# Kernel optimization log

Hardware: AMD Instinct MI355X
Metric: run time of the kernel (lower is better)

The kernel has to match this reference:

```python
import jax, jax.numpy as jnp
import numpy as np

B, S, V, D, H, DK, DH, L = 1, 2048, 256, 1024, 16, 64, 4096, 4
EPS = 1e-5
SCALE = 1.0 / np.sqrt(DK)


def _ln(x, g, b):
    mu = jnp.mean(x, axis=-1, keepdims=True)
    var = jnp.mean(jnp.square(x - mu), axis=-1, keepdims=True)
    return (x - mu) * jax.lax.rsqrt(var + EPS) * g + b


def setup_inputs() -> dict:
    key = jax.random.key(0)
    ks = jax.random.split(key, 20)
    f = lambda k, shape: (0.02 * jax.random.normal(k, shape)).astype(jnp.float32)
    return {
        "x": jax.random.randint(ks[0], (B, S), 0, V),
        "emb": f(ks[1], (V, D)),
        "pos": f(ks[2], (S, D)),
        "Wq": f(ks[3], (L, D, H * DK)), "bq": jnp.zeros((L, H * DK), jnp.float32),
        "Wk": f(ks[4], (L, D, H * DK)), "bk": jnp.zeros((L, H * DK), jnp.float32),
        "Wv": f(ks[5], (L, D, H * DK)), "bv": jnp.zeros((L, H * DK), jnp.float32),
        "Wo": f(ks[6], (L, H * DK, D)),
        "ln1_g": jnp.ones((L, D), jnp.float32), "ln1_b": jnp.zeros((L, D), jnp.float32),
        "W1": f(ks[7], (L, D, DH)), "b1": jnp.zeros((L, DH), jnp.float32),
        "W2": f(ks[8], (L, DH, D)), "b2": jnp.zeros((L, D), jnp.float32),
        "ln2_g": jnp.ones((L, D), jnp.float32), "ln2_b": jnp.zeros((L, D), jnp.float32),
        "head_w": f(ks[9], (D, V)), "head_b": jnp.zeros((V,), jnp.float32),
    }


def _forward(x, emb, pos, Wq, bq, Wk, bk, Wv, bv, Wo, ln1_g, ln1_b,
             W1, b1, W2, b2, ln2_g, ln2_b, head_w, head_b):
    h = emb[x] + pos[:S]                      # [B,S,D]
    causal = jnp.tril(jnp.ones((S, S), bool))  # additive -inf above diag
    for i in range(L):
        # --- naive attention: explicit QK^T, mask, softmax, @V ---
        q = (h @ Wq[i] + bq[i]).reshape(B, S, H, DK)
        k = (h @ Wk[i] + bk[i]).reshape(B, S, H, DK)
        v = (h @ Wv[i] + bv[i]).reshape(B, S, H, DK)
        scores = jnp.einsum('bqhd,bkhd->bhqk', q * SCALE, k)   # [B,H,S,S]
        scores = jnp.where(causal[None, None], scores, -jnp.inf)
        p = jax.nn.softmax(scores, axis=-1)
        a = jnp.einsum('bhqk,bkhd->bqhd', p, v).reshape(B, S, H * DK) @ Wo[i]
        # --- TransformerLayer: x + ln2(mlp(x + ln1(attn(x)))) ---
        u = h + _ln(a, ln1_g[i], ln1_b[i])
        m = jax.nn.gelu(u @ W1[i] + b1[i], approximate=False) @ W2[i] + b2[i]
        h = h + _ln(m, ln2_g[i], ln2_b[i])
    return h @ head_w + head_b                 # [B,S,V]


def reference(x, emb, pos, Wq, bq, Wk, bk, Wv, bv, Wo, ln1_g, ln1_b,
              W1, b1, W2, b2, ln2_g, ln2_b, head_w, head_b):
    return _forward(x, emb, pos, Wq, bq, Wk, bk, Wv, bv, Wo, ln1_g, ln1_b,
                    W1, b1, W2, b2, ln2_g, ln2_b, head_w, head_b)
```

## Files before the change

kernel.cpp:

```cpp
#include <hip/hip_runtime.h>
#include <hip/hip_bf16.h>
#include <cstdint>
#include <math.h>

static constexpr int S_  = 2048;
static constexpr int D_  = 1024;
static constexpr int H_  = 16;
static constexpr int DK_ = 64;
static constexpr int DH_ = 4096;
static constexpr int L_  = 4;
static constexpr int V_  = 256;
#define ATT_SCALE 0.125f

typedef __bf16 bf16;
typedef __bf16 bf16x8 __attribute__((ext_vector_type(8)));
typedef __bf16 bf16x4v __attribute__((ext_vector_type(4)));
typedef float  f32x4  __attribute__((ext_vector_type(4)));

__device__ __forceinline__ __attribute__((address_space(3))) void* to_lds(const void* p) {
  return (__attribute__((address_space(3))) void*)(uintptr_t)p;
}
__device__ __forceinline__ __attribute__((address_space(1))) void* to_glb(const void* p) {
  return (__attribute__((address_space(1))) void*)(uintptr_t)p;
}

template <int TN, int SPLIT, int GELU_EPI>
__device__ __forceinline__ void gemm_body(
    const bf16* __restrict__ A, const bf16* __restrict__ Bt,
    const float* __restrict__ bias, float* __restrict__ Cf, bf16* __restrict__ Cb,
    float* __restrict__ P0, float* __restrict__ P1,
    int M, int N, int K)
{
  constexpr int BU = TN / 32;
  constexpr int JN = TN / 32;
  __shared__ __align__(16) bf16 sA[2][128 * 64];
  __shared__ __align__(16) bf16 sB[2][TN * 64];
  const int tid  = threadIdx.x;
  const int wave = tid >> 6;
  const int lane = tid & 63;
  const int l16  = lane & 15;
  const int quad = lane >> 4;

  const int idl = blockIdx.y * 16 + blockIdx.x;
  const int qch = (gridDim.x * gridDim.y) >> 3;
  const int wsw = (idl & 7) * qch + (idl >> 3);
  const int bm  = (wsw & 15) * 128;
  const int bn  = (wsw >> 4) * TN;

  const int wm = (wave & 1) * 64;
  const int wn = (wave >> 1) * (TN / 2);

  const int KS = K / SPLIT;
  const size_t kofs = (SPLIT > 1) ? (size_t)blockIdx.z * KS : 0;

  const int srow = tid >> 3;
  const int sc8  = (tid & 7) ^ (srow & 7);
  const bf16* gA = A  + (size_t)(bm + srow) * K + kofs + sc8 * 8;
  const bf16* gB = Bt + (size_t)(bn + srow) * K + kofs + sc8 * 8;

  const int swz = l16 & 7;

  f32x4 acc[4][JN] = {};

#pragma unroll
  for (int u = 0; u < 4; ++u)
    __builtin_amdgcn_global_load_lds(to_glb(gA + (size_t)u * 32 * K),
                                     to_lds(&sA[0][u * 2048 + tid * 8]), 16, 0, 0);
#pragma unroll
  for (int u = 0; u < BU; ++u)
    __builtin_amdgcn_global_load_lds(to_glb(gB + (size_t)u * 32 * K),
                                     to_lds(&sB[0][u * 2048 + tid * 8]), 16, 0, 0);

  int cur = 0;
  for (int k0 = 0; k0 < KS; k0 += 64, cur ^= 1) {
    if (k0 + 64 < KS) {
      const int nb = cur ^ 1;
      const size_t ko = k0 + 64;
#pragma unroll
      for (int u = 0; u < 4; ++u)
        __builtin_amdgcn_global_load_lds(to_glb(gA + ko + (size_t)u * 32 * K),
                                         to_lds(&sA[nb][u * 2048 + tid * 8]), 16, 0, 0);
#pragma unroll
      for (int u = 0; u < BU; ++u)
        __builtin_amdgcn_global_load_lds(to_glb(gB + ko + (size_t)u * 32 * K),
                                         to_lds(&sB[nb][u * 2048 + tid * 8]), 16, 0, 0);
      if constexpr (BU == 4) asm volatile("s_waitcnt vmcnt(8)" ::: "memory");
      else                   asm volatile("s_waitcnt vmcnt(6)" ::: "memory");
    } else {
      asm volatile("s_waitcnt vmcnt(0)" ::: "memory");
    }
    __builtin_amdgcn_s_barrier();

    bf16x8 af[2][4], bfv[2][JN];
#pragma unroll
    for (int kc = 0; kc < 2; ++kc) {
      const int c8 = ((kc * 4 + quad) ^ swz) * 8;
#pragma unroll
      for (int i = 0; i < 4; ++i)
        af[kc][i] = *(const bf16x8*)&sA[cur][(wm + i * 16 + l16) * 64 + c8];
#pragma unroll
      for (int j = 0; j < JN; ++j)
        bfv[kc][j] = *(const bf16x8*)&sB[cur][(wn + j * 16 + l16) * 64 + c8];
    }
    asm volatile("s_waitcnt lgkmcnt(0)" ::: "memory");
    __builtin_amdgcn_s_barrier();

#pragma unroll
    for (int kc = 0; kc < 2; ++kc)
#pragma unroll
      for (int i = 0; i < 4; ++i)
#pragma unroll
        for (int j = 0; j < JN; ++j)
          acc[i][j] = __builtin_amdgcn_mfma_f32_16x16x32_bf16(af[kc][i], bfv[kc][j], acc[i][j], 0, 0, 0);
  }

  if constexpr (SPLIT > 1) {
    float* Pf;
    if constexpr (SPLIT == 4)
      Pf = (blockIdx.z < 2) ? (P0 + (size_t)blockIdx.z * ((size_t)M * N))
                            : (P1 + (size_t)(blockIdx.z - 2) * ((size_t)M * N));
    else
      Pf = (blockIdx.z == 0) ? P0 : P1;
#pragma unroll
    for (int i = 0; i < 4; ++i)
#pragma unroll
      for (int j = 0; j < JN; ++j) {
        const int col = bn + wn + j * 16 + l16;
#pragma unroll
        for (int r = 0; r < 4; ++r) {
          const int row = bm + wm + i * 16 + quad * 4 + r;
          Pf[(size_t)row * N + col] = acc[i][j][r];
        }
      }
  } else {
#pragma unroll
    for (int i = 0; i < 4; ++i) {
#pragma unroll
      for (int j = 0; j < JN; ++j) {
        const int col = bn + wn + j * 16 + l16;
        const float bz = bias ? bias[col] : 0.0f;
#pragma unroll
        for (int r = 0; r < 4; ++r) {
          const int row = bm + wm + i * 16 + quad * 4 + r;
          float v = acc[i][j][r] + bz;
          if (GELU_EPI) v = 0.5f * v * (1.0f + erff(v * 0.70710678118654752f));
          if (Cf) Cf[(size_t)row * N + col] = v;
          if (Cb) Cb[(size_t)row * N + col] = (bf16)v;
        }
      }
    }
  }
}

__global__ __launch_bounds__(256) void gemm_qkv_kernel(
    const bf16* __restrict__ A, const bf16* __restrict__ Bt,
    const float* __restrict__ bias, bf16* __restrict__ Cb, int M, int N, int K)
{ gemm_body<64, 1, 0>(A, Bt, bias, nullptr, Cb, nullptr, nullptr, M, N, K); }

__global__ __launch_bounds__(256) void gemm_wo_kernel(
    const bf16* __restrict__ A, const bf16* __restrict__ Bt,
    float* __restrict__ P0, float* __restrict__ P1, int M, int N, int K)
{ gemm_body<128, 2, 0>(A, Bt, nullptr, nullptr, nullptr, P0, P1, M, N, K); }

__global__ __launch_bounds__(256) void gemm_mlp1_kernel(
    const bf16* __restrict__ A, const bf16* __restrict__ Bt,
    const float* __restrict__ bias, bf16* __restrict__ Cb, int M, int N, int K)
{ gemm_body<64, 1, 1>(A, Bt, bias, nullptr, Cb, nullptr, nullptr, M, N, K); }

__global__ __launch_bounds__(256) void gemm_mlp2_kernel(
    const bf16* __restrict__ A, const bf16* __restrict__ Bt,
    float* __restrict__ P0, float* __restrict__ P1, int M, int N, int K)
{ gemm_body<128, 4, 0>(A, Bt, nullptr, nullptr, nullptr, P0, P1, M, N, K); }

__global__ __launch_bounds__(256) void gemm_head_kernel(
    const bf16* __restrict__ A, const bf16* __restrict__ Bt,
    float* __restrict__ P0, float* __restrict__ P1, int M, int N, int K)
{ gemm_body<64, 4, 0>(A, Bt, nullptr, nullptr, nullptr, P0, P1, M, N, K); }

__global__ __launch_bounds__(256) void splitk_reduce4_kernel(
    const float* __restrict__ P0, const float* __restrict__ P1,
    const float* __restrict__ bias, float* __restrict__ Cf, size_t MN, int N)
{
  const size_t i = ((size_t)blockIdx.x * 256 + threadIdx.x) * 4;
  const float4 a = *(const float4*)(P0 + i);
  const float4 b = *(const float4*)(P0 + MN + i);
  const float4 c = *(const float4*)(P1 + i);
  const float4 d = *(const float4*)(P1 + MN + i);
  float4 o;
  o.x = a.x + b.x + c.x + d.x; o.y = a.y + b.y + c.y + d.y;
  o.z = a.z + b.z + c.z + d.z; o.w = a.w + b.w + c.w + d.w;
  const int col = (int)(i & (size_t)(N - 1));
  const float4 bz = *(const float4*)(bias + col);
  o.x += bz.x; o.y += bz.y; o.z += bz.z; o.w += bz.w;
  *(float4*)(Cf + i) = o;
}

__device__ __forceinline__ float wave_reduce_sum(float v) {
#pragma unroll
  for (int off = 32; off > 0; off >>= 1) v += __shfl_xor(v, off, 64);
  return v;
}

template <int SPLIT>
__device__ __forceinline__ void ln_fused_body(
    const float* __restrict__ P0, const float* __restrict__ P1,
    const float* __restrict__ bias, const float* __restrict__ resid,
    const float* __restrict__ g, const float* __restrict__ b,
    float* __restrict__ outf, bf16* __restrict__ outb, size_t MN)
{
  const int r = blockIdx.x;
  const int t = threadIdx.x;
  const size_t ro = (size_t)r * D_;
  float4 x;
  {
    const float4 a0 = ((const float4*)(P0 + ro))[t];
    float4 a1;
    if constexpr (SPLIT == 2) a1 = ((const float4*)(P1 + ro))[t];
    else                      a1 = ((const float4*)(P0 + MN + ro))[t];
    x.x = a0.x + a1.x; x.y = a0.y + a1.y; x.z = a0.z + a1.z; x.w = a0.w + a1.w;
    if constexpr (SPLIT == 4) {
      const float4 a2 = ((const float4*)(P1 + ro))[t];
      const float4 a3 = ((const float4*)(P1 + MN + ro))[t];
      x.x += a2.x + a3.x; x.y += a2.y + a3.y; x.z += a2.z + a3.z; x.w += a2.w + a3.w;
    }
  }
  if (bias) {
    const float4 bz = ((const float4*)bias)[t];
    x.x += bz.x; x.y += bz.y; x.z += bz.z; x.w += bz.w;
  }
  float s  = x.x + x.y + x.z + x.w;
  float s2 = x.x * x.x + x.y * x.y + x.z * x.z + x.w * x.w;
  s  = wave_reduce_sum(s);
  s2 = wave_reduce_sum(s2);
  __shared__ float red[8];
  const int wave = t >> 6, lane = t & 63;
  if (lane == 0) { red[wave] = s; red[4 + wave] = s2; }
  __syncthreads();
  s  = red[0] + red[1] + red[2] + red[3];
  s2 = red[4] + red[5] + red[6] + red[7];
  const float mu  = s * (1.0f / 1024.0f);
  const float var = s2 * (1.0f / 1024.0f) - mu * mu;
  const float rs  = rsqrtf(var + 1e-5f);
  const float4 gv = ((const float4*)g)[t];
  const float4 bv = ((const float4*)b)[t];
  const float4 hv = ((const float4*)(resid + ro))[t];
  const float o0 = hv.x + (x.x - mu) * rs * gv.x + bv.x;
  const float o1 = hv.y + (x.y - mu) * rs * gv.y + bv.y;
  const float o2 = hv.z + (x.z - mu) * rs * gv.z + bv.z;
  const float o3 = hv.w + (x.w - mu) * rs * gv.w + bv.w;
  if (outf) { float4 o4; o4.x = o0; o4.y = o1; o4.z = o2; o4.w = o3;
              ((float4*)(outf + ro))[t] = o4; }
  if (outb) { bf16x4v ob = {(bf16)o0, (bf16)o1, (bf16)o2, (bf16)o3};
              ((bf16x4v*)(outb + ro))[t] = ob; }
}

__global__ __launch_bounds__(256) void ln_fused2_kernel(
    const float* __restrict__ P0, const float* __restrict__ P1,
    const float* __restrict__ resid, const float* __restrict__ g,
    const float* __restrict__ b, bf16* __restrict__ outb, size_t MN)
{ ln_fused_body<2>(P0, P1, nullptr, resid, g, b, nullptr, outb, MN); }

__global__ __launch_bounds__(256) void ln_fused4_kernel(
    const float* __restrict__ P0, const float* __restrict__ P1,
    const float* __restrict__ bias, const float* __restrict__ resid,
    const float* __restrict__ g, const float* __restrict__ b,
    float* __restrict__ outf, bf16* __restrict__ outb, size_t MN)
{ ln_fused_body<4>(P0, P1, bias, resid, g, b, outf, outb, MN); }

__device__ __forceinline__ void transpose_tile(
    const float* __restrict__ in, bf16* __restrict__ out, int K, int N)
{
  __shared__ float t[32][33];
  const int k0 = blockIdx.y * 32;
  const int n0 = blockIdx.x * 32;
  const int tx = threadIdx.x & 31;
  const int ty = threadIdx.x >> 5;
#pragma unroll
  for (int i = 0; i < 32; i += 8)
    t[ty + i][tx] = in[(size_t)(k0 + ty + i) * N + (n0 + tx)];
  __syncthreads();
#pragma unroll
  for (int i = 0; i < 32; i += 8)
    out[(size_t)(n0 + ty + i) * K + (k0 + tx)] = (bf16)t[tx][ty + i];
}

__global__ __launch_bounds__(256) void transpose_cast_kernel(
    const float* __restrict__ in, bf16* __restrict__ out, int K, int N)
{ transpose_tile(in, out, K, N); }

__global__ __launch_bounds__(256) void transpose_all_kernel(
    const float* __restrict__ in, bf16* __restrict__ out, int K, int N,
    size_t in_stride, size_t out_stride)
{
  transpose_tile(in + (size_t)blockIdx.z * in_stride,
                 out + (size_t)blockIdx.z * out_stride, K, N);
}

__global__ __launch_bounds__(256) void transpose_qkv_all_kernel(
    const float* __restrict__ Wq, const float* __restrict__ Wk, const float* __restrict__ Wv,
    bf16* __restrict__ out)
{
  const int z = blockIdx.z;
  const int layer = z / 3, which = z % 3;
  const float* in = (which == 0) ? Wq : (which == 1) ? Wk : Wv;
  transpose_tile(in + (size_t)layer * D_ * D_,
                 out + ((size_t)layer * 3 + which) * D_ * D_, D_, D_);
}

__global__ __launch_bounds__(256) void vtrans_kernel(
    const bf16* __restrict__ qkv, bf16* __restrict__ vT)
{
  __shared__ bf16 t[32][65];
  const int s0 = blockIdx.x * 32;
  const int head = blockIdx.y;
  const int sr = threadIdx.x >> 3, d8 = (threadIdx.x & 7) * 8;
  bf16x8 v = *(const bf16x8*)(qkv + (size_t)(s0 + sr) * (3 * D_) + 2 * D_ + head * DK_ + d8);
#pragma unroll
  for (int i = 0; i < 8; ++i) t[sr][d8 + i] = v[i];
  __syncthreads();
  const int dw = threadIdx.x >> 2, s4 = (threadIdx.x & 3) * 8;
  bf16x8 o;
#pragma unroll
  for (int i = 0; i < 8; ++i) o[i] = t[s4 + i][dw];
  *(bf16x8*)(vT + (size_t)head * DK_ * S_ + (size_t)dw * S_ + s0 + s4) = o;
}

__global__ __launch_bounds__(256) void embed_kernel(
    const int* __restrict__ x, const float* __restrict__ emb, const float* __restrict__ pos,
    float* __restrict__ hf, bf16* __restrict__ hb)
{
  const int s = blockIdx.x;
  const int d = threadIdx.x * 4;
  const int tok = x[s];
  const float4 e = *(const float4*)(emb + (size_t)tok * D_ + d);
  const float4 p = *(const float4*)(pos + (size_t)s * D_ + d);
  float4 o; o.x = e.x + p.x; o.y = e.y + p.y; o.z = e.z + p.z; o.w = e.w + p.w;
  *(float4*)(hf + (size_t)s * D_ + d) = o;
  bf16x4v ob = {(bf16)o.x, (bf16)o.y, (bf16)o.z, (bf16)o.w};
  *(bf16x4v*)(hb + (size_t)s * D_ + d) = ob;
}

__global__ __launch_bounds__(256) void attn_mfma_kernel(
    const bf16* __restrict__ qkv, const bf16* __restrict__ vT, bf16* __restrict__ out)
{
  __shared__ __align__(16) bf16 sK[2][64 * 64];
  __shared__ __align__(16) bf16 sV[2][64 * 64];
  __shared__ __align__(16) bf16 sP[4][16 * 64];

  const int head = blockIdx.y;
  const int xb   = blockIdx.x;
  const int qIdx = (head & 8) ? (31 - xb) : xb;
  const int qb   = qIdx * 64;
  const int tid  = threadIdx.x;
  const int wave = tid >> 6, lane = tid & 63;
  const int l16  = lane & 15, quad = lane >> 4;
  const int swz  = l16 & 7;

  const size_t rstr = 3 * D_;
  const bf16* kbase = qkv + D_ + head * DK_;
  const bf16* vbase = vT + (size_t)head * DK_ * S_;

  const int srow   = tid >> 3;
  const int kchunk = (tid & 7) ^ (srow & 7);

  bf16x8 aq0, aq1;
  {
    const bf16* qrow = qkv + (size_t)(qb + wave * 16 + l16) * rstr + head * DK_ + quad * 8;
    bf16x8 t0 = *(const bf16x8*)(qrow);
    bf16x8 t1 = *(const bf16x8*)(qrow + 32);
#pragma unroll
    for (int i = 0; i < 8; ++i) {
      aq0[i] = (bf16)((float)t0[i] * ATT_SCALE);
      aq1[i] = (bf16)((float)t1[i] * ATT_SCALE);
    }
  }

  f32x4 oa[4] = {};
  float lsum[4] = {0.0f, 0.0f, 0.0f, 0.0f};
  const int qrow0 = qb + wave * 16 + quad * 4;
  const int jmax = qb + 63;

#pragma unroll
  for (int u = 0; u < 2; ++u) {
    const int r = u * 32 + srow;
    __builtin_amdgcn_global_load_lds(to_glb(kbase + (size_t)r * rstr + kchunk * 8),
                                     to_lds(&sK[0][u * 2048 + tid * 8]), 16, 0, 0);
    __builtin_amdgcn_global_load_lds(to_glb(vbase + (size_t)r * S_ + kchunk * 8),
                                     to_lds(&sV[0][u * 2048 + tid * 8]), 16, 0, 0);
  }

  int cur = 0;
  for (int j0 = 0; j0 <= jmax; j0 += 64, cur ^= 1) {
    if (j0 + 64 <= jmax) {
      const int nb = cur ^ 1;
      const int jn = j0 + 64;
#pragma unroll
      for (int u = 0; u < 2; ++u) {
        const int r = u * 32 + srow;
        __builtin_amdgcn_global_load_lds(to_glb(kbase + (size_t)(jn + r) * rstr + kchunk * 8),
                                         to_lds(&sK[nb][u * 2048 + tid * 8]), 16, 0, 0);
        __builtin_amdgcn_global_load_lds(to_glb(vbase + (size_t)r * S_ + jn + kchunk * 8),
                                         to_lds(&sV[nb][u * 2048 + tid * 8]), 16, 0, 0);
      }
      asm volatile("s_waitcnt vmcnt(4)" ::: "memory");
    } else {
      asm volatile("s_waitcnt vmcnt(0)" ::: "memory");
    }
    __builtin_amdgcn_s_barrier();

    f32x4 sc[4];
#pragma unroll
    for (int n = 0; n < 4; ++n) {
      const bf16* kr = &sK[cur][(n * 16 + l16) * 64];
      bf16x8 bk0 = *(const bf16x8*)(kr + ((quad    ) ^ swz) * 8);
      bf16x8 bk1 = *(const bf16x8*)(kr + ((quad + 4) ^ swz) * 8);
      f32x4 z = {};
      z = __builtin_amdgcn_mfma_f32_16x16x32_bf16(aq0, bk0, z, 0, 0, 0);
      z = __builtin_amdgcn_mfma_f32_16x16x32_bf16(aq1, bk1, z, 0, 0, 0);
      sc[n] = z;
    }
    bf16 pb[4][4];
#pragma unroll
    for (int n = 0; n < 4; ++n) {
      const int key = j0 + n * 16 + l16;
#pragma unroll
      for (int r = 0; r < 4; ++r) {
        const float p = (key <= qrow0 + r) ? __expf(sc[n][r]) : 0.0f;
        lsum[r] += p;
        pb[n][r] = (bf16)p;
      }
    }
    bf16* pw = &sP[wave][0];
    const int cb = l16 >> 3, co = l16 & 7;
#pragma unroll
    for (int n = 0; n < 4; ++n) {
#pragma unroll
      for (int r = 0; r < 4; ++r) {
        const int row = quad * 4 + r;
        const int ch = (2 * n + cb) ^ (row & 7);
        pw[row * 64 + ch * 8 + co] = pb[n][r];
      }
    }
    asm volatile("s_waitcnt lgkmcnt(0)" ::: "memory");
    __builtin_amdgcn_wave_barrier();
    bf16x8 ap0 = *(const bf16x8*)&pw[l16 * 64 + ((quad    ) ^ swz) * 8];
    bf16x8 ap1 = *(const bf16x8*)&pw[l16 * 64 + ((quad + 4) ^ swz) * 8];

#pragma unroll
    for (int n = 0; n < 4; ++n) {
      const bf16* vr = &sV[cur][(n * 16 + l16) * 64];
      bf16x8 bv0 = *(const bf16x8*)(vr + ((quad    ) ^ swz) * 8);
      bf16x8 bv1 = *(const bf16x8*)(vr + ((quad + 4) ^ swz) * 8);
      oa[n] = __builtin_amdgcn_mfma_f32_16x16x32_bf16(ap0, bv0, oa[n], 0, 0, 0);
      oa[n] = __builtin_amdgcn_mfma_f32_16x16x32_bf16(ap1, bv1, oa[n], 0, 0, 0);
    }
    asm volatile("s_waitcnt lgkmcnt(0)" ::: "memory");
    __builtin_amdgcn_s_barrier();
  }

#pragma unroll
  for (int r = 0; r < 4; ++r) {
#pragma unroll
    for (int off = 1; off <= 8; off <<= 1)
      lsum[r] += __shfl_xor(lsum[r], off, 64);
  }
#pragma unroll
  for (int r = 0; r < 4; ++r) {
    const float inv = 1.0f / lsum[r];
    const int qrow = qrow0 + r;
#pragma unroll
    for (int n = 0; n < 4; ++n)
      out[(size_t)qrow * D_ + head * DK_ + n * 16 + l16] = (bf16)(oa[n][r] * inv);
  }
}

__global__ __launch_bounds__(256) void pack3_all_kernel(
    const float* __restrict__ a, const float* __restrict__ b, const float* __restrict__ c,
    float* __restrict__ out)
{
  const int i = blockIdx.x * 256 + threadIdx.x;
  const int l = blockIdx.y;
  float v;
  if (i < 1024) v = a[l * 1024 + i];
  else if (i < 2048) v = b[l * 1024 + i - 1024];
  else v = c[l * 1024 + i - 2048];
  out[(size_t)l * 3072 + i] = v;
}

extern "C" void kernel_launch(void* const* d_in, const int* in_sizes, int n_in,
                              void* d_out, int out_size, void* d_ws, size_t ws_size,
                              hipStream_t stream)
{
  const int*   x     = (const int*)d_in[0];
  const float* emb   = (const float*)d_in[1];
  const float* pos   = (const float*)d_in[2];
  const float* Wq    = (const float*)d_in[3];
  const float* bq    = (const float*)d_in[4];
  const float* Wk    = (const float*)d_in[5];
  const float* bk    = (const float*)d_in[6];
  const float* Wv    = (const float*)d_in[7];
  const float* bv    = (const float*)d_in[8];
  const float* Wo    = (const float*)d_in[9];
  const float* ln1g  = (const float*)d_in[10];
  const float* ln1b  = (const float*)d_in[11];
  const float* W1    = (const float*)d_in[12];
  const float* b1    = (const float*)d_in[13];
  const float* W2    = (const float*)d_in[14];
  const float* b2    = (const float*)d_in[15];
  const float* ln2g  = (const float*)d_in[16];
  const float* ln2b  = (const float*)d_in[17];
  const float* headw = (const float*)d_in[18];
  const float* headb = (const float*)d_in[19];

  char* w = (char*)d_ws;
  float* h_f32   = (float*)w;  w += (size_t)S_ * D_ * 4;
  bf16*  h_b     = (bf16*)w;   w += (size_t)S_ * D_ * 2;
  bf16*  qkv_b   = (bf16*)w;   w += (size_t)S_ * 3 * D_ * 2;
  bf16*  attn_b  = (bf16*)w;   w += (size_t)S_ * D_ * 2;
  float* a_f32   = (float*)w;  w += (size_t)S_ * D_ * 4;
  bf16*  u_b     = (bf16*)w;   w += (size_t)S_ * D_ * 2;
  bf16*  mh_b    = (bf16*)w;   w += (size_t)S_ * DH_ * 2;
  float* m_f32   = (float*)w;  w += (size_t)S_ * D_ * 4;
  float* scr     = (float*)w;  w += (size_t)32 << 20;
  bf16*  qkvT_a  = (bf16*)w;   w += (size_t)L_ * 3 * D_ * D_ * 2;
  bf16*  woT_a   = (bf16*)w;   w += (size_t)L_ * D_ * D_ * 2;
  bf16*  w1T_a   = (bf16*)w;   w += (size_t)L_ * DH_ * D_ * 2;
  bf16*  w2T_a   = (bf16*)w;   w += (size_t)L_ * D_ * DH_ * 2;
  bf16*  headT   = (bf16*)w;   w += (size_t)V_ * D_ * 2;
  float* qkvbias = (float*)w;  w += (size_t)L_ * 3 * D_ * 4;
  bf16* vT = qkvT_a;

  float* m2P0 = scr;
  float* m2P1 = scr + ((size_t)4 << 20);
  float* hP0  = scr;
  float* hP1  = scr + ((size_t)1 << 20);

  embed_kernel<<<dim3(S_), dim3(256), 0, stream>>>(x, emb, pos, h_f32, h_b);
  pack3_all_kernel<<<dim3(12, L_), dim3(256), 0, stream>>>(bq, bk, bv, qkvbias);
  transpose_qkv_all_kernel<<<dim3(D_ / 32, D_ / 32, 3 * L_), dim3(256), 0, stream>>>(
      Wq, Wk, Wv, qkvT_a);
  transpose_all_kernel<<<dim3(D_ / 32, D_ / 32, L_), dim3(256), 0, stream>>>(
      Wo, woT_a, D_, D_, (size_t)D_ * D_, (size_t)D_ * D_);
  transpose_all_kernel<<<dim3(DH_ / 32, D_ / 32, L_), dim3(256), 0, stream>>>(
      W1, w1T_a, D_, DH_, (size_t)D_ * DH_, (size_t)DH_ * D_);
  transpose_all_kernel<<<dim3(D_ / 32, DH_ / 32, L_), dim3(256), 0, stream>>>(
      W2, w2T_a, DH_, D_, (size_t)DH_ * D_, (size_t)D_ * DH_);
  transpose_cast_kernel<<<dim3(V_ / 32, D_ / 32), dim3(256), 0, stream>>>(headw, headT, D_, V_);

  for (int i = 0; i < L_; ++i) {
    const bf16* qkvT_i = qkvT_a + (size_t)i * 3 * D_ * D_;
    const bf16* woT_i  = woT_a  + (size_t)i * D_ * D_;
    const bf16* w1T_i  = w1T_a  + (size_t)i * DH_ * D_;
    const bf16* w2T_i  = w2T_a  + (size_t)i * D_ * DH_;

    gemm_qkv_kernel<<<dim3(S_ / 128, 3 * D_ / 64), dim3(256), 0, stream>>>(
        h_b, qkvT_i, qkvbias + (size_t)i * 3 * D_, qkv_b, S_, 3 * D_, D_);
    vtrans_kernel<<<dim3(S_ / 32, H_), dim3(256), 0, stream>>>(qkv_b, vT);
    attn_mfma_kernel<<<dim3(S_ / 64, H_), dim3(256), 0, stream>>>(qkv_b, vT, attn_b);
    gemm_wo_kernel<<<dim3(S_ / 128, D_ / 128, 2), dim3(256), 0, stream>>>(
        attn_b, woT_i, a_f32, m_f32, S_, D_, D_);
    ln_fused2_kernel<<<dim3(S_), dim3(256), 0, stream>>>(
        a_f32, m_f32, h_f32, ln1g + (size_t)i * D_, ln1b + (size_t)i * D_, u_b, (size_t)S_ * D_);
    gemm_mlp1_kernel<<<dim3(S_ / 128, DH_ / 64), dim3(256), 0, stream>>>(
        u_b, w1T_i, b1 + (size_t)i * DH_, mh_b, S_, DH_, D_);
    gemm_mlp2_kernel<<<dim3(S_ / 128, D_ / 128, 4), dim3(256), 0, stream>>>(
        mh_b, w2T_i, m2P0, m2P1, S_, D_, DH_);
    ln_fused4_kernel<<<dim3(S_), dim3(256), 0, stream>>>(
        m2P0, m2P1, b2 + (size_t)i * D_, h_f32, ln2g + (size_t)i * D_, ln2b + (size_t)i * D_,
        h_f32, h_b, (size_t)S_ * D_);
  }

  gemm_head_kernel<<<dim3(S_ / 128, V_ / 64, 4), dim3(256), 0, stream>>>(
      h_b, headT, hP0, hP1, S_, V_, D_);
  splitk_reduce4_kernel<<<dim3((unsigned)((size_t)S_ * V_ / 1024)), dim3(256), 0, stream>>>(
      hP0, hP1, headb, (float*)d_out, (size_t)S_ * V_, V_);
}
```

Measured before the change: 846.9 us.

## Use 256x256 8-wave ping-pong GEMM for QKV and MLP1 projections

Replaces the 128x64-tile GEMM used for the QKV and MLP-up projections with a new 512-thread kernel computing 256x256 output tiles. It uses double-buffered direct global-to-LDS loads split into quarter-phases interleaved with MFMA work, plus priority raising around the MFMA bursts. Larger tiles raise arithmetic intensity and cut global traffic. The cost is far fewer blocks (96 for QKV, 128 for MLP1), which may underfill the 256 CUs, and heavy LDS and register use that limits occupancy.

```diff
diff --git a/kernel.cpp b/kernel.cpp
--- a/kernel.cpp
+++ b/kernel.cpp
@@ -23,6 +23,131 @@
 __device__ __forceinline__ __attribute__((address_space(1))) void* to_glb(const void* p) {
   return (__attribute__((address_space(1))) void*)(uintptr_t)p;
 }
+
+template <int GELU>
+__device__ __forceinline__ void gemm8p_body(
+    const bf16* __restrict__ A, const bf16* __restrict__ Bt,
+    const float* __restrict__ bias, bf16* __restrict__ Cb,
+    int M, int N, int K)
+{
+  __shared__ __align__(16) bf16 sA[2][2][128 * 64];
+  __shared__ __align__(16) bf16 sB[2][2][128 * 64];
+  const int tid  = threadIdx.x;
+  const int wave = tid >> 6, lane = tid & 63;
+  const int l16  = lane & 15, quad = lane >> 4;
+  const int wr   = wave >> 2;
+  const int wc   = wave & 3;
+  const int bm   = blockIdx.x * 256;
+  const int bn   = blockIdx.y * 256;
+  const int wm   = wr * 128, wn = wc * 64;
+  const int srow = tid >> 3;
+  const int sc8  = (tid & 7) ^ (srow & 7);
+  const int swz  = l16 & 7;
+  const int tid8 = tid * 8;
+
+  const bf16* gA = A  + (size_t)(bm + srow) * K + sc8 * 8;
+  const bf16* gB = Bt + (size_t)(bn + srow) * K + sc8 * 8;
+
+  f32x4 acc[8][4] = {};
+  bf16x8 bfv[2][4];
+
+#define SA8(b,h,u,t) __builtin_amdgcn_global_load_lds( \
+    to_glb(gA + (size_t)((h)*128 + (u)*64) * K + (size_t)(t) * 64), \
+    to_lds(&sA[b][h][(u)*4096 + tid8]), 16, 0, 0)
+#define SB8(b,h,u,t) __builtin_amdgcn_global_load_lds( \
+    to_glb(gB + (size_t)((h)*128 + (u)*64) * K + (size_t)(t) * 64), \
+    to_lds(&sB[b][h][(u)*4096 + tid8]), 16, 0, 0)
+#define AG0(b,t) { SA8(b,0,0,t); SA8(b,1,0,t); }
+#define AG1(b,t) { SA8(b,0,1,t); SA8(b,1,1,t); }
+#define BH0(b,t) { SB8(b,0,0,t); SB8(b,0,1,t); }
+#define BH1(b,t) { SB8(b,1,0,t); SB8(b,1,1,t); }
+
+#define PHASE8(b, q, READB, STAGE, WAIT) do { \
+    bf16x8 af[2][2]; \
+    _Pragma("unroll") \
+    for (int kc = 0; kc < 2; ++kc) { \
+      const int c8 = ((kc * 4 + quad) ^ swz) * 8; \
+      af[kc][0] = *(const bf16x8*)&sA[b][wr][((q) * 32      + l16) * 64 + c8]; \
+      af[kc][1] = *(const bf16x8*)&sA[b][wr][((q) * 32 + 16 + l16) * 64 + c8]; \
+      if (READB) { \
+        _Pragma("unroll") \
+        for (int n = 0; n < 4; ++n) \
+          bfv[kc][n] = *(const bf16x8*)&sB[b][wc >> 1][((wc & 1) * 64 + n * 16 + l16) * 64 + c8]; \
+      } \
+    } \
+    STAGE; WAIT; \
+    __builtin_amdgcn_s_barrier(); \
+    asm volatile("s_waitcnt lgkmcnt(0)" ::: "memory"); \
+    __builtin_amdgcn_s_setprio(1); \
+    _Pragma("unroll") \
+    for (int kc = 0; kc < 2; ++kc) \
+      _Pragma("unroll") \
+      for (int mm = 0; mm < 2; ++mm) \
+        _Pragma("unroll") \
+        for (int n = 0; n < 4; ++n) \
+          acc[(q) * 2 + mm][n] = __builtin_amdgcn_mfma_f32_16x16x32_bf16( \
+              af[kc][mm], bfv[kc][n], acc[(q) * 2 + mm][n], 0, 0, 0); \
+    __builtin_amdgcn_s_setprio(0); \
+    __builtin_amdgcn_s_barrier(); \
+  } while (0)
+
+  const int NT2 = K >> 7;
+
+  BH0(0, 0); BH1(0, 0); AG0(0, 0); AG1(0, 0);
+  BH0(1, 1); BH1(1, 1); AG0(1, 1);
+  asm volatile("s_waitcnt vmcnt(6)" ::: "memory");
+  __builtin_amdgcn_s_barrier();
+
+  for (int i2 = 0; i2 < NT2; ++i2) {
+    const int t1 = 2 * i2 + 1, t2 = 2 * i2 + 2, t3 = 2 * i2 + 3;
+    const bool more = (i2 + 1 < NT2);
+    PHASE8(0, 0, 1, { AG1(1, t1); }, {});
+    PHASE8(0, 1, 0, { if (more) BH0(0, t2); }, {});
+    PHASE8(0, 2, 0, { if (more) BH1(0, t2); }, {});
+    PHASE8(0, 3, 0, { if (more) AG0(0, t2); },
+           { if (more) asm volatile("s_waitcnt vmcnt(6)" ::: "memory");
+             else      asm volatile("s_waitcnt vmcnt(0)" ::: "memory"); });
+    PHASE8(1, 0, 1, { if (more) AG1(0, t2); }, {});
+    PHASE8(1, 1, 0, { if (more) BH0(1, t3); }, {});
+    PHASE8(1, 2, 0, { if (more) BH1(1, t3); }, {});
+    PHASE8(1, 3, 0, { if (more) AG0(1, t3); },
+           { if (more) asm volatile("s_waitcnt vmcnt(6)" ::: "memory"); });
+  }
+
+#undef PHASE8
+#undef AG0
+#undef AG1
+#undef BH0
+#undef BH1
+#undef SA8
+#undef SB8
+
+#pragma unroll
+  for (int m = 0; m < 8; ++m) {
+#pragma unroll
+    for (int n = 0; n < 4; ++n) {
+      const int col = bn + wn + n * 16 + l16;
+      const float bz = bias ? bias[col] : 0.0f;
+#pragma unroll
+      for (int r = 0; r < 4; ++r) {
+        const int row = bm + wm + m * 16 + quad * 4 + r;
+        float v = acc[m][n][r] + bz;
+        if (GELU) v = 0.5f * v * (1.0f + erff(v * 0.70710678118654752f));
+        Cb[(size_t)row * N + col] = (bf16)v;
+      }
+    }
+  }
+}
+
+__global__ __launch_bounds__(512) void gemm8p_qkv_kernel(
+    const bf16* __restrict__ A, const bf16* __restrict__ Bt,
+    const float* __restrict__ bias, bf16* __restrict__ Cb, int M, int N, int K)
+{ gemm8p_body<0>(A, Bt, bias, Cb, M, N, K); }
+
+__global__ __launch_bounds__(512) void gemm8p_gelu_kernel(
+    const bf16* __restrict__ A, const bf16* __restrict__ Bt,
+    const float* __restrict__ bias, bf16* __restrict__ Cb, int M, int N, int K)
+{ gemm8p_body<1>(A, Bt, bias, Cb, M, N, K); }
 
 template <int TN, int SPLIT, int GELU_EPI>
 __device__ __forceinline__ void gemm_body(
@@ -152,20 +277,10 @@
   }
 }
 
-__global__ __launch_bounds__(256) void gemm_qkv_kernel(
-    const bf16* __restrict__ A, const bf16* __restrict__ Bt,
-    const float* __restrict__ bias, bf16* __restrict__ Cb, int M, int N, int K)
-{ gemm_body<64, 1, 0>(A, Bt, bias, nullptr, Cb, nullptr, nullptr, M, N, K); }
-
 __global__ __launch_bounds__(256) void gemm_wo_kernel(
     const bf16* __restrict__ A, const bf16* __restrict__ Bt,
     float* __restrict__ P0, float* __restrict__ P1, int M, int N, int K)
 { gemm_body<128, 2, 0>(A, Bt, nullptr, nullptr, nullptr, P0, P1, M, N, K); }
-
-__global__ __launch_bounds__(256) void gemm_mlp1_kernel(
-    const bf16* __restrict__ A, const bf16* __restrict__ Bt,
-    const float* __restrict__ bias, bf16* __restrict__ Cb, int M, int N, int K)
-{ gemm_body<64, 1, 1>(A, Bt, bias, nullptr, Cb, nullptr, nullptr, M, N, K); }
 
 __global__ __launch_bounds__(256) void gemm_mlp2_kernel(
     const bf16* __restrict__ A, const bf16* __restrict__ Bt,
@@ -553,7 +668,7 @@
     const bf16* w1T_i  = w1T_a  + (size_t)i * DH_ * D_;
     const bf16* w2T_i  = w2T_a  + (size_t)i * D_ * DH_;
 
-    gemm_qkv_kernel<<<dim3(S_ / 128, 3 * D_ / 64), dim3(256), 0, stream>>>(
+    gemm8p_qkv_kernel<<<dim3(S_ / 256, 3 * D_ / 256), dim3(512), 0, stream>>>(
         h_b, qkvT_i, qkvbias + (size_t)i * 3 * D_, qkv_b, S_, 3 * D_, D_);
     vtrans_kernel<<<dim3(S_ / 32, H_), dim3(256), 0, stream>>>(qkv_b, vT);
     attn_mfma_kernel<<<dim3(S_ / 64, H_), dim3(256), 0, stream>>>(qkv_b, vT, attn_b);
@@ -561,7 +676,7 @@
         attn_b, woT_i, a_f32, m_f32, S_, D_, D_);
     ln_fused2_kernel<<<dim3(S_), dim3(256), 0, stream>>>(
         a_f32, m_f32, h_f32, ln1g + (size_t)i * D_, ln1b + (size_t)i * D_, u_b, (size_t)S_ * D_);
-    gemm_mlp1_kernel<<<dim3(S_ / 128, DH_ / 64), dim3(256), 0, stream>>>(
+    gemm8p_gelu_kernel<<<dim3(S_ / 256, DH_ / 256), dim3(512), 0, stream>>>(
         u_b, w1T_i, b1 + (size_t)i * DH_, mh_b, S_, DH_, D_);
     gemm_mlp2_kernel<<<dim3(S_ / 128, D_ / 128, 4), dim3(256), 0, stream>>>(
         mh_b, w2T_i, m2P0, m2P1, S_, D_, DH_);
```

Result: slower. 956.6 us (+13.0%).

## Fuse V transpose into QKV GEMM epilogue and retile MLP2 split-K

Applied to the files above, without the earlier changes.

The QKV GEMM epilogue now writes the V third of its output straight into a per-head transposed layout, so the separate vtrans kernel launch and its extra read/write pass over V are gone. The MLP2 GEMM moves from 128-wide tiles with 4-way split-K to 64-wide tiles with 2-way split-K. Its partials now land in the a_f32/m_f32 buffers and are reduced by a single LN kernel that optionally adds bias. The transposed V stores are strided and uncoalesced, and halving the split-K depth doubles the K length per block.

```diff
diff --git a/kernel.cpp b/kernel.cpp
--- a/kernel.cpp
+++ b/kernel.cpp
@@ -24,11 +24,11 @@
   return (__attribute__((address_space(1))) void*)(uintptr_t)p;
 }
 
-template <int TN, int SPLIT, int GELU_EPI>
+template <int TN, int SPLIT, int GELU_EPI, int VOUT>
 __device__ __forceinline__ void gemm_body(
     const bf16* __restrict__ A, const bf16* __restrict__ Bt,
     const float* __restrict__ bias, float* __restrict__ Cf, bf16* __restrict__ Cb,
-    float* __restrict__ P0, float* __restrict__ P1,
+    float* __restrict__ P0, float* __restrict__ P1, bf16* __restrict__ Vt,
     int M, int N, int K)
 {
   constexpr int BU = TN / 32;
@@ -133,6 +133,24 @@
         }
       }
   } else {
+    if constexpr (VOUT) {
+      if (bn >= 2 * D_) {
+        bf16* vb = Vt + (size_t)((bn - 2 * D_) >> 6) * DK_ * S_;
+#pragma unroll
+        for (int i = 0; i < 4; ++i)
+#pragma unroll
+          for (int j = 0; j < JN; ++j) {
+            const int d  = wn + j * 16 + l16;
+            const float bz = bias[bn + d];
+#pragma unroll
+            for (int r = 0; r < 4; ++r) {
+              const int row = bm + wm + i * 16 + quad * 4 + r;
+              vb[(size_t)d * S_ + row] = (bf16)(acc[i][j][r] + bz);
+            }
+          }
+        return;
+      }
+    }
 #pragma unroll
     for (int i = 0; i < 4; ++i) {
 #pragma unroll
@@ -154,28 +172,29 @@
 
 __global__ __launch_bounds__(256) void gemm_qkv_kernel(
     const bf16* __restrict__ A, const bf16* __restrict__ Bt,
-    const float* __restrict__ bias, bf16* __restrict__ Cb, int M, int N, int K)
-{ gemm_body<64, 1, 0>(A, Bt, bias, nullptr, Cb, nullptr, nullptr, M, N, K); }
+    const float* __restrict__ bias, bf16* __restrict__ Cb, bf16* __restrict__ Vt,
+    int M, int N, int K)
+{ gemm_body<64, 1, 0, 1>(A, Bt, bias, nullptr, Cb, nullptr, nullptr, Vt, M, N, K); }
 
 __global__ __launch_bounds__(256) void gemm_wo_kernel(
     const bf16* __restrict__ A, const bf16* __restrict__ Bt,
     float* __restrict__ P0, float* __restrict__ P1, int M, int N, int K)
-{ gemm_body<128, 2, 0>(A, Bt, nullptr, nullptr, nullptr, P0, P1, M, N, K); }
+{ gemm_body<128, 2, 0, 0>(A, Bt, nullptr, nullptr, nullptr, P0, P1, nullptr, M, N, K); }
 
 __global__ __launch_bounds__(256) void gemm_mlp1_kernel(
     const bf16* __restrict__ A, const bf16* __restrict__ Bt,
     const float* __restrict__ bias, bf16* __restrict__ Cb, int M, int N, int K)
-{ gemm_body<64, 1, 1>(A, Bt, bias, nullptr, Cb, nullptr, nullptr, M, N, K); }
+{ gemm_body<64, 1, 1, 0>(A, Bt, bias, nullptr, Cb, nullptr, nullptr, nullptr, M, N, K); }
 
 __global__ __launch_bounds__(256) void gemm_mlp2_kernel(
     const bf16* __restrict__ A, const bf16* __restrict__ Bt,
     float* __restrict__ P0, float* __restrict__ P1, int M, int N, int K)
-{ gemm_body<128, 4, 0>(A, Bt, nullptr, nullptr, nullptr, P0, P1, M, N, K); }
+{ gemm_body<64, 2, 0, 0>(A, Bt, nullptr, nullptr, nullptr, P0, P1, nullptr, M, N, K); }
 
 __global__ __launch_bounds__(256) void gemm_head_kernel(
     const bf16* __restrict__ A, const bf16* __restrict__ Bt,
     float* __restrict__ P0, float* __restrict__ P1, int M, int N, int K)
-{ gemm_body<64, 4, 0>(A, Bt, nullptr, nullptr, nullptr, P0, P1, M, N, K); }
+{ gemm_body<64, 4, 0, 0>(A, Bt, nullptr, nullptr, nullptr, P0, P1, nullptr, M, N, K); }
 
 __global__ __launch_bounds__(256) void splitk_reduce4_kernel(
     const float* __restrict__ P0, const float* __restrict__ P1,
@@ -256,16 +275,10 @@
 
 __global__ __launch_bounds__(256) void ln_fused2_kernel(
     const float* __restrict__ P0, const float* __restrict__ P1,
-    const float* __restrict__ resid, const float* __restrict__ g,
-    const float* __restrict__ b, bf16* __restrict__ outb, size_t MN)
-{ ln_fused_body<2>(P0, P1, nullptr, resid, g, b, nullptr, outb, MN); }
-
-__global__ __launch_bounds__(256) void ln_fused4_kernel(
-    const float* __restrict__ P0, const float* __restrict__ P1,
     const float* __restrict__ bias, const float* __restrict__ resid,
     const float* __restrict__ g, const float* __restrict__ b,
     float* __restrict__ outf, bf16* __restrict__ outb, size_t MN)
-{ ln_fused_body<4>(P0, P1, bias, resid, g, b, outf, outb, MN); }
+{ ln_fused_body<2>(P0, P1, bias, resid, g, b, outf, outb, MN); }
 
 __device__ __forceinline__ void transpose_tile(
     const float* __restrict__ in, bf16* __restrict__ out, int K, int N)
@@ -305,24 +318,6 @@
   const float* in = (which == 0) ? Wq : (which == 1) ? Wk : Wv;
   transpose_tile(in + (size_t)layer * D_ * D_,
                  out + ((size_t)layer * 3 + which) * D_ * D_, D_, D_);
-}
-
-__global__ __launch_bounds__(256) void vtrans_kernel(
-    const bf16* __restrict__ qkv, bf16* __restrict__ vT)
-{
-  __shared__ bf16 t[32][65];
-  const int s0 = blockIdx.x * 32;
-  const int head = blockIdx.y;
-  const int sr = threadIdx.x >> 3, d8 = (threadIdx.x & 7) * 8;
-  bf16x8 v = *(const bf16x8*)(qkv + (size_t)(s0 + sr) * (3 * D_) + 2 * D_ + head * DK_ + d8);
-#pragma unroll
-  for (int i = 0; i < 8; ++i) t[sr][d8 + i] = v[i];
-  __syncthreads();
-  const int dw = threadIdx.x >> 2, s4 = (threadIdx.x & 3) * 8;
-  bf16x8 o;
-#pragma unroll
-  for (int i = 0; i < 8; ++i) o[i] = t[s4 + i][dw];
-  *(bf16x8*)(vT + (size_t)head * DK_ * S_ + (size_t)dw * S_ + s0 + s4) = o;
 }
 
 __global__ __launch_bounds__(256) void embed_kernel(
@@ -528,12 +523,10 @@
   bf16*  w2T_a   = (bf16*)w;   w += (size_t)L_ * D_ * DH_ * 2;
   bf16*  headT   = (bf16*)w;   w += (size_t)V_ * D_ * 2;
   float* qkvbias = (float*)w;  w += (size_t)L_ * 3 * D_ * 4;
-  bf16* vT = qkvT_a;
-
-  float* m2P0 = scr;
-  float* m2P1 = scr + ((size_t)4 << 20);
-  float* hP0  = scr;
-  float* hP1  = scr + ((size_t)1 << 20);
+
+  bf16* vT = (bf16*)scr;
+  float* hP0 = scr;
+  float* hP1 = scr + ((size_t)1 << 20);
 
   embed_kernel<<<dim3(S_), dim3(256), 0, stream>>>(x, emb, pos, h_f32, h_b);
   pack3_all_kernel<<<dim3(12, L_), dim3(256), 0, stream>>>(bq, bk, bv, qkvbias);
@@ -554,19 +547,19 @@
     const bf16* w2T_i  = w2T_a  + (size_t)i * D_ * DH_;
 
     gemm_qkv_kernel<<<dim3(S_ / 128, 3 * D_ / 64), dim3(256), 0, stream>>>(
-        h_b, qkvT_i, qkvbias + (size_t)i * 3 * D_, qkv_b, S_, 3 * D_, D_);
-    vtrans_kernel<<<dim3(S_ / 32, H_), dim3(256), 0, stream>>>(qkv_b, vT);
+        h_b, qkvT_i, qkvbias + (size_t)i * 3 * D_, qkv_b, vT, S_, 3 * D_, D_);
     attn_mfma_kernel<<<dim3(S_ / 64, H_), dim3(256), 0, stream>>>(qkv_b, vT, attn_b);
     gemm_wo_kernel<<<dim3(S_ / 128, D_ / 128, 2), dim3(256), 0, stream>>>(
         attn_b, woT_i, a_f32, m_f32, S_, D_, D_);
     ln_fused2_kernel<<<dim3(S_), dim3(256), 0, stream>>>(
-        a_f32, m_f32, h_f32, ln1g + (size_t)i * D_, ln1b + (size_t)i * D_, u_b, (size_t)S_ * D_);
+        a_f32, m_f32, nullptr, h_f32, ln1g + (size_t)i * D_, ln1b + (size_t)i * D_,
+        nullptr, u_b, (size_t)S_ * D_);
     gemm_mlp1_kernel<<<dim3(S_ / 128, DH_ / 64), dim3(256), 0, stream>>>(
         u_b, w1T_i, b1 + (size_t)i * DH_, mh_b, S_, DH_, D_);
-    gemm_mlp2_kernel<<<dim3(S_ / 128, D_ / 128, 4), dim3(256), 0, stream>>>(
-        mh_b, w2T_i, m2P0, m2P1, S_, D_, DH_);
-    ln_fused4_kernel<<<dim3(S_), dim3(256), 0, stream>>>(
-        m2P0, m2P1, b2 + (size_t)i * D_, h_f32, ln2g + (size_t)i * D_, ln2b + (size_t)i * D_,
+    gemm_mlp2_kernel<<<dim3(S_ / 128, D_ / 64, 2), dim3(256), 0, stream>>>(
+        mh_b, w2T_i, a_f32, m_f32, S_, D_, DH_);
+    ln_fused2_kernel<<<dim3(S_), dim3(256), 0, stream>>>(
+        a_f32, m_f32, b2 + (size_t)i * D_, h_f32, ln2g + (size_t)i * D_, ln2b + (size_t)i * D_,
         h_f32, h_b, (size_t)S_ * D_);
   }
 
```

After: 806.3 us. -4.8%, faster.
